# Optimization experiments

Measured on AMD Instinct MI355X. Metric: run time of the kernel, lower is better.

## Reference

```python
import jax, jax.numpy as jnp
import numpy as np

HIDDEN = 1024
HEADS = 16
HEAD_DIM = HIDDEN // HEADS
SCALE = float(np.sqrt(HEAD_DIM))


def setup_inputs() -> dict:
    key = jax.random.key(0)
    ks = jax.random.split(key, 9)
    B, S = 4, 8192
    std = 1.0 / np.sqrt(HIDDEN)
    x = jax.random.normal(ks[0], (B, S, HIDDEN), dtype=jnp.float32)
    Wq = jax.random.normal(ks[1], (HIDDEN, HIDDEN), dtype=jnp.float32) * std
    Wk = jax.random.normal(ks[2], (HIDDEN, HIDDEN), dtype=jnp.float32) * std
    Wv = jax.random.normal(ks[3], (HIDDEN, HIDDEN), dtype=jnp.float32) * std
    Wo = jax.random.normal(ks[4], (HIDDEN, HIDDEN), dtype=jnp.float32) * std
    bq = jax.random.normal(ks[5], (HIDDEN,), dtype=jnp.float32) * std
    bk = jax.random.normal(ks[6], (HIDDEN,), dtype=jnp.float32) * std
    bv = jax.random.normal(ks[7], (HIDDEN,), dtype=jnp.float32) * std
    bo = jax.random.normal(ks[8], (HIDDEN,), dtype=jnp.float32) * std
    return {"x": x, "Wq": Wq, "bq": bq, "Wk": Wk, "bk": bk,
            "Wv": Wv, "bv": bv, "Wo": Wo, "bo": bo}


def reference(x, Wq, bq, Wk, bk, Wv, bv, Wo, bo):
    B, S, E = x.shape
    H, D = HEADS, HEAD_DIM
    # torch nn.Linear: y = x @ W^T + b
    q = (jnp.einsum('bse,fe->bsf', x, Wq) + bq).reshape(B, S, H, D)
    k = (jnp.einsum('bse,fe->bsf', x, Wk) + bk).reshape(B, S, H, D)
    v = (jnp.einsum('bse,fe->bsf', x, Wv) + bv).reshape(B, S, H, D)
    # Faithful to source: NO head transpose, so matmul contracts over head_dim
    # with (B,S) as batch dims -> per-token head-mixing scores [B,S,H,H].
    scores = jnp.einsum('bshd,bsgd->bshg', q, k) / SCALE
    probs = jax.nn.softmax(scores, axis=-1)
    attn = jnp.einsum('bshg,bsgd->bshd', probs, v).reshape(B, S, E)
    return jnp.einsum('bse,fe->bsf', attn, Wo) + bo
```

## Files before the change

kernel.cpp:

```cpp
#include <hip/hip_runtime.h>
#include <hip/hip_bf16.h>
#include <cstdint>
#include <type_traits>

#define GLOBAL_AS __attribute__((address_space(1)))
#define LDS_AS    __attribute__((address_space(3)))

typedef short bf16x8 __attribute__((ext_vector_type(8)));
typedef short short8_t __attribute__((ext_vector_type(8)));
typedef float f32x4  __attribute__((ext_vector_type(4)));

static constexpr int E_DIM = 1024;
static constexpr int HD = 64;
static constexpr int QKV_STRIDE = 3072;
static constexpr int KDIM = 1024;
static constexpr int NTK  = KDIM / 64;
static constexpr int NIT  = NTK / 2;

__device__ __forceinline__ float b2f(short s) {
    union { unsigned u; float f; } x;
    x.u = ((unsigned)(unsigned short)s) << 16;
    return x.f;
}
__device__ __forceinline__ short f2b(float f) {
    union { float f; unsigned u; } x; x.f = f;
    unsigned r = x.u + 0x7FFF + ((x.u >> 16) & 1);
    return (short)(r >> 16);
}

__global__ __launch_bounds__(256) void k_prep(
    const float* __restrict__ x,
    const float* __restrict__ Wq, const float* __restrict__ Wk,
    const float* __restrict__ Wv, const float* __restrict__ Wo,
    const float* __restrict__ bq, const float* __restrict__ bk,
    const float* __restrict__ bv,
    short* __restrict__ xb, short* __restrict__ Wqkvb, short* __restrict__ Wob,
    float* __restrict__ bqkv, int n4x, int n4w)
{
    int i = blockIdx.x * 256 + threadIdx.x;
    const float* src;
    short* dst;
    int j;
    if (i < n4x)                       { src = x;  dst = xb;                  j = i; }
    else if (i < n4x + n4w)            { src = Wq; dst = Wqkvb;               j = i - n4x; }
    else if (i < n4x + 2 * n4w)        { src = Wk; dst = Wqkvb + 4 * n4w;     j = i - n4x - n4w; }
    else if (i < n4x + 3 * n4w)        { src = Wv; dst = Wqkvb + 8 * n4w;     j = i - n4x - 2 * n4w; }
    else if (i < n4x + 4 * n4w)        { src = Wo; dst = Wob;                 j = i - n4x - 3 * n4w; }
    else {
        int b = i - (n4x + 4 * n4w);
        if (b < 768) {
            #pragma unroll
            for (int e = 0; e < 4; ++e) {
                int idx = b * 4 + e;
                float v = (idx < 1024) ? bq[idx] : (idx < 2048 ? bk[idx - 1024] : bv[idx - 2048]);
                bqkv[idx] = v;
            }
        }
        return;
    }
    float4 v = reinterpret_cast<const float4*>(src)[j];
    short4 o;
    o.x = f2b(v.x); o.y = f2b(v.y); o.z = f2b(v.z); o.w = f2b(v.w);
    reinterpret_cast<short4*>(dst)[j] = o;
}

template <typename OutT>
__global__ __launch_bounds__(512, 2) void k_gemm256(
    const short* __restrict__ A,
    const short* __restrict__ Bm,
    const float* __restrict__ bias,
    OutT* __restrict__ C,
    int NT_N, int N)
{
    __shared__ short lds[65536];

    const int tid  = threadIdx.x;
    const int lane = tid & 63;
    const int wv   = tid >> 6;
    const int wr   = wv >> 2;
    const int wc   = wv & 3;
    const int frow = lane & 15;
    const int ks   = lane >> 4;
    const int sw   = frow & 7;
    const int sl0  = ((0 + ks) ^ sw) * 8;
    const int sl1  = ((4 + ks) ^ sw) * 8;

    const int nwg = gridDim.x, nper = nwg >> 3, bid = blockIdx.x;
    const int swz = (bid & 7) * nper + (bid >> 3);
    const int m0  = (swz / NT_N) * 256;
    const int n0  = (swz % NT_N) * 256;

    const int ArdBase = wr * 8192;
    const int BrdBase = 16384 + (wc >> 1) * 8192 + (wc & 1) * 4096;

    const int srow = tid >> 3;
    const int ssl  = ((tid & 7) ^ (srow & 7)) * 8;
    const int sdst = tid * 8;

#define GLD(SRC, DST) __builtin_amdgcn_global_load_lds(                            \
        (const GLOBAL_AS short*)(SRC), (LDS_AS short*)(DST), 16, 0, 0)
#define STAGE_A(BUF, HALF, T) do {                                                 \
    const short* s_ = A + (size_t)(m0 + (HALF) * 128 + srow) * KDIM + (T) * 64 + ssl; \
    short* d_ = &lds[(BUF) * 32768 + (HALF) * 8192 + sdst];                        \
    GLD(s_, d_);  GLD(s_ + (size_t)64 * KDIM, d_ + 4096);                          \
} while (0)
#define STAGE_B(BUF, HALF, T) do {                                                 \
    const short* s_ = Bm + (size_t)(n0 + (HALF) * 128 + srow) * KDIM + (T) * 64 + ssl; \
    short* d_ = &lds[(BUF) * 32768 + 16384 + (HALF) * 8192 + sdst];                \
    GLD(s_, d_);  GLD(s_ + (size_t)64 * KDIM, d_ + 4096);                          \
} while (0)

#define RD_A(BUF, MIB) do {                                                        \
    _Pragma("unroll")                                                              \
    for (int m_ = 0; m_ < 4; ++m_) {                                               \
        const short* p_ = &lds[(BUF) * 32768 + ArdBase + ((MIB) + m_) * 1024 + frow * 64]; \
        af[m_][0] = *(const bf16x8*)(p_ + sl0);                                    \
        af[m_][1] = *(const bf16x8*)(p_ + sl1);                                    \
    }                                                                              \
} while (0)
#define RD_B(BUF, NIB, BF) do {                                                    \
    _Pragma("unroll")                                                              \
    for (int n_ = 0; n_ < 2; ++n_) {                                               \
        const short* p_ = &lds[(BUF) * 32768 + BrdBase + ((NIB) + n_) * 1024 + frow * 64]; \
        BF[n_][0] = *(const bf16x8*)(p_ + sl0);                                    \
        BF[n_][1] = *(const bf16x8*)(p_ + sl1);                                    \
    }                                                                              \
} while (0)

#define MM(MB, NB, BF) do {                                                        \
    _Pragma("unroll")                                                              \
    for (int m_ = 0; m_ < 4; ++m_)                                                 \
        _Pragma("unroll")                                                          \
        for (int n_ = 0; n_ < 2; ++n_) {                                           \
            acc[(MB)+m_][(NB)+n_] = __builtin_amdgcn_mfma_f32_16x16x32_bf16(       \
                af[m_][0], BF[n_][0], acc[(MB)+m_][(NB)+n_], 0, 0, 0);             \
            acc[(MB)+m_][(NB)+n_] = __builtin_amdgcn_mfma_f32_16x16x32_bf16(       \
                af[m_][1], BF[n_][1], acc[(MB)+m_][(NB)+n_], 0, 0, 0);             \
        }                                                                          \
} while (0)

#define BAR   do { __builtin_amdgcn_s_barrier();                                   \
                   __builtin_amdgcn_sched_barrier(0); } while (0)
#define VM8   asm volatile("s_waitcnt vmcnt(8)" ::: "memory")
#define PRIO1 __builtin_amdgcn_s_setprio(1)
#define PRIO0 __builtin_amdgcn_s_setprio(0)

    f32x4 acc[8][4];
    #pragma unroll
    for (int i = 0; i < 8; ++i)
        #pragma unroll
        for (int j = 0; j < 4; ++j)
            acc[i][j] = (f32x4){0.f, 0.f, 0.f, 0.f};

    bf16x8 af[4][2], bfA[2][2], bfB[2][2];

    STAGE_A(0, 0, 0);  STAGE_B(0, 0, 0);  STAGE_B(0, 1, 0);  STAGE_A(0, 1, 0);
    STAGE_B(1, 0, 1);  STAGE_B(1, 1, 1);
    STAGE_A(1, 0, 1);  STAGE_A(1, 1, 1);
    VM8;  BAR;

    #pragma unroll 1
    for (int it = 0; it < NIT; ++it) {
        const int tb = (2 * it + 2 <= 15) ? 2 * it + 2 : 15;
        const int tc = (2 * it + 3 <= 15) ? 2 * it + 3 : 15;
        const int bb = tb & 1, bc = tc & 1;

        RD_A(0, 0);  RD_B(0, 0, bfA);
        BAR;
        PRIO1;  MM(0, 0, bfA);  PRIO0;  BAR;
        RD_B(0, 2, bfB);
        BAR;
        PRIO1;  MM(0, 2, bfB);  PRIO0;  BAR;
        RD_A(0, 4);
        STAGE_B(bb, 0, tb);  STAGE_B(bb, 1, tb);
        BAR;
        PRIO1;  MM(4, 0, bfA);  PRIO0;  BAR;
        STAGE_A(bb, 0, tb);  STAGE_A(bb, 1, tb);
        BAR;
        PRIO1;  MM(4, 2, bfB);  PRIO0;
        VM8;  BAR;

        RD_A(1, 0);  RD_B(1, 0, bfA);
        BAR;
        PRIO1;  MM(0, 0, bfA);  PRIO0;  BAR;
        RD_B(1, 2, bfB);
        BAR;
        PRIO1;  MM(0, 2, bfB);  PRIO0;  BAR;
        RD_A(1, 4);
        STAGE_B(bc, 0, tc);  STAGE_B(bc, 1, tc);
        BAR;
        PRIO1;  MM(4, 0, bfA);  PRIO0;  BAR;
        STAGE_A(bc, 0, tc);  STAGE_A(bc, 1, tc);
        BAR;
        PRIO1;  MM(4, 2, bfB);  PRIO0;
        VM8;  BAR;
    }

    asm volatile("s_waitcnt vmcnt(0)" ::: "memory");

    const int crow = (lane >> 4) * 4;
    const int ccol = lane & 15;
    float bv4[4];
    #pragma unroll
    for (int ni = 0; ni < 4; ++ni)
        bv4[ni] = bias[n0 + wc * 64 + ni * 16 + ccol];
    #pragma unroll
    for (int mi = 0; mi < 8; ++mi) {
        #pragma unroll
        for (int r = 0; r < 4; ++r) {
            const size_t rowg = (size_t)(m0 + wr * 128 + mi * 16 + crow + r) * N;
            #pragma unroll
            for (int ni = 0; ni < 4; ++ni) {
                const int col = n0 + wc * 64 + ni * 16 + ccol;
                float v = acc[mi][ni][r] + bv4[ni];
                if constexpr (std::is_same<OutT, float>::value) {
                    C[rowg + col] = v;
                } else {
                    C[rowg + col] = f2b(v);
                }
            }
        }
    }
#undef GLD
#undef STAGE_A
#undef STAGE_B
#undef RD_A
#undef RD_B
#undef MM
#undef BAR
#undef VM8
#undef PRIO1
#undef PRIO0
}

__global__ __launch_bounds__(256) void k_attn(
    const short* __restrict__ QKV, short* __restrict__ O)
{
    __shared__ short Ks[16][1032];
    __shared__ short Vs[16][1032];

    const int tid = threadIdx.x;
    const int tok0 = blockIdx.x * 16;

    for (int i = tid; i < 2048; i += 256) {
        int t = i >> 7;
        int j = i & 127;
        const size_t base = (size_t)(tok0 + t) * QKV_STRIDE;
        *reinterpret_cast<short8_t*>(&Ks[t][j * 8]) =
            *reinterpret_cast<const short8_t*>(&QKV[base + 1024 + j * 8]);
        *reinterpret_cast<short8_t*>(&Vs[t][j * 8]) =
            *reinterpret_cast<const short8_t*>(&QKV[base + 2048 + j * 8]);
    }
    __syncthreads();

    const int tl = tid >> 4;
    const int h  = tid & 15;

    float qf[64];
    const short* qp = QKV + (size_t)(tok0 + tl) * QKV_STRIDE + h * HD;
    #pragma unroll
    for (int i = 0; i < 8; ++i) {
        short8_t v = *reinterpret_cast<const short8_t*>(&qp[i * 8]);
        #pragma unroll
        for (int j = 0; j < 8; ++j) qf[i * 8 + j] = b2f(v[j]);
    }

    float s[16];
    #pragma unroll
    for (int g = 0; g < 16; ++g) {
        float a = 0.f;
        #pragma unroll
        for (int i = 0; i < 8; ++i) {
            short8_t kv = *reinterpret_cast<const short8_t*>(&Ks[tl][g * HD + i * 8]);
            #pragma unroll
            for (int j = 0; j < 8; ++j) a += qf[i * 8 + j] * b2f(kv[j]);
        }
        s[g] = a * 0.125f;
    }
    float mx = s[0];
    #pragma unroll
    for (int g = 1; g < 16; ++g) mx = fmaxf(mx, s[g]);
    float l = 0.f;
    #pragma unroll
    for (int g = 0; g < 16; ++g) { s[g] = __expf(s[g] - mx); l += s[g]; }
    const float inv = 1.f / l;
    #pragma unroll
    for (int g = 0; g < 16; ++g) s[g] *= inv;

    short* op = O + (size_t)(tok0 + tl) * E_DIM + h * HD;
    #pragma unroll
    for (int c = 0; c < 4; ++c) {
        float a[16];
        #pragma unroll
        for (int j = 0; j < 16; ++j) a[j] = 0.f;
        #pragma unroll
        for (int g = 0; g < 16; ++g) {
            short8_t v0 = *reinterpret_cast<const short8_t*>(&Vs[tl][g * HD + c * 16]);
            short8_t v1 = *reinterpret_cast<const short8_t*>(&Vs[tl][g * HD + c * 16 + 8]);
            #pragma unroll
            for (int j = 0; j < 8; ++j) {
                a[j]     += s[g] * b2f(v0[j]);
                a[8 + j] += s[g] * b2f(v1[j]);
            }
        }
        short8_t o0, o1;
        #pragma unroll
        for (int j = 0; j < 8; ++j) { o0[j] = f2b(a[j]); o1[j] = f2b(a[8 + j]); }
        *reinterpret_cast<short8_t*>(&op[c * 16])     = o0;
        *reinterpret_cast<short8_t*>(&op[c * 16 + 8]) = o1;
    }
}

extern "C" void kernel_launch(void* const* d_in, const int* in_sizes, int n_in,
                              void* d_out, int out_size, void* d_ws, size_t ws_size,
                              hipStream_t stream) {
    const float* x  = (const float*)d_in[0];
    const float* Wq = (const float*)d_in[1];
    const float* bq = (const float*)d_in[2];
    const float* Wk = (const float*)d_in[3];
    const float* bk = (const float*)d_in[4];
    const float* Wv = (const float*)d_in[5];
    const float* bv = (const float*)d_in[6];
    const float* Wo = (const float*)d_in[7];
    const float* bo = (const float*)d_in[8];
    float* out = (float*)d_out;

    const int T = in_sizes[0] / E_DIM;
    char* ws = (char*)d_ws;
    const size_t SZ_X    = (size_t)T * E_DIM * 2;
    const size_t SZ_WQKV = (size_t)3 * E_DIM * E_DIM * 2;
    const size_t SZ_W    = (size_t)E_DIM * E_DIM * 2;
    const size_t SZ_B    = 3072 * sizeof(float) + 4096;

    short* xb    = (short*)(ws);
    short* Wqkvb = (short*)(ws + SZ_X);
    short* Wob   = (short*)(ws + SZ_X + SZ_WQKV);
    float* bqkv  = (float*)(ws + SZ_X + SZ_WQKV + SZ_W);
    short* QKVb  = (short*)(ws + SZ_X + SZ_WQKV + SZ_W + SZ_B);
    short* Ab    = xb;

    const int n4x = T * E_DIM / 4;
    const int n4w = E_DIM * E_DIM / 4;
    const int nprep = n4x + 4 * n4w + 768;
    k_prep<<<dim3((nprep + 255) / 256), dim3(256), 0, stream>>>(
        x, Wq, Wk, Wv, Wo, bq, bk, bv, xb, Wqkvb, Wob, bqkv, n4x, n4w);

    k_gemm256<short><<<dim3((T / 256) * (QKV_STRIDE / 256)), dim3(512), 0, stream>>>(
        xb, Wqkvb, bqkv, QKVb, QKV_STRIDE / 256, QKV_STRIDE);

    k_attn<<<dim3(T / 16), dim3(256), 0, stream>>>(QKVb, Ab);

    k_gemm256<float><<<dim3((T / 256) * (E_DIM / 256)), dim3(512), 0, stream>>>(
        Ab, Wob, bo, out, E_DIM / 256, E_DIM);
}
```

Baseline: 407.6 us.

## Restagger GEMM global-to-LDS prefetch schedule with finer-grained waitcnt control

Reorders the GEMM main loop so A tiles are staged one step later and interleaved with B staging across the four MFMA phases, reducing outstanding loads from 8 to 4 per sync point. Removes sched_barrier from BAR and adds explicit lgkmcnt waits so LDS reads can overlap with barriers. The aim is to spread memory traffic more evenly across compute phases and cut stall time at barriers. In exchange, the compiler gets more scheduling freedom and the hand-tuned buffer-reuse ordering must stay race-free.

```diff
diff --git a/kernel.cpp b/kernel.cpp
--- a/kernel.cpp
+++ b/kernel.cpp
@@ -139,9 +139,10 @@
         }                                                                          \
 } while (0)
 
-#define BAR   do { __builtin_amdgcn_s_barrier();                                   \
-                   __builtin_amdgcn_sched_barrier(0); } while (0)
-#define VM8   asm volatile("s_waitcnt vmcnt(8)" ::: "memory")
+#define BAR   __builtin_amdgcn_s_barrier()
+#define LGKM0 asm volatile("s_waitcnt lgkmcnt(0)")
+#define LGKM8 asm volatile("s_waitcnt lgkmcnt(8)")
+#define VM4   asm volatile("s_waitcnt vmcnt(4)" ::: "memory")
 #define PRIO1 __builtin_amdgcn_s_setprio(1)
 #define PRIO0 __builtin_amdgcn_s_setprio(0)
 
@@ -154,46 +155,50 @@
 
     bf16x8 af[4][2], bfA[2][2], bfB[2][2];
 
-    STAGE_A(0, 0, 0);  STAGE_B(0, 0, 0);  STAGE_B(0, 1, 0);  STAGE_A(0, 1, 0);
+    STAGE_B(0, 0, 0);  STAGE_B(0, 1, 0);
+    STAGE_A(0, 0, 0);  STAGE_A(0, 1, 0);
     STAGE_B(1, 0, 1);  STAGE_B(1, 1, 1);
-    STAGE_A(1, 0, 1);  STAGE_A(1, 1, 1);
-    VM8;  BAR;
+    VM4;  BAR;
 
     #pragma unroll 1
     for (int it = 0; it < NIT; ++it) {
+        const int ta = 2 * it + 1;
         const int tb = (2 * it + 2 <= 15) ? 2 * it + 2 : 15;
         const int tc = (2 * it + 3 <= 15) ? 2 * it + 3 : 15;
-        const int bb = tb & 1, bc = tc & 1;
 
         RD_A(0, 0);  RD_B(0, 0, bfA);
-        BAR;
+        STAGE_A(1, 0, ta);
+        LGKM8;  BAR;  LGKM0;
         PRIO1;  MM(0, 0, bfA);  PRIO0;  BAR;
         RD_B(0, 2, bfB);
-        BAR;
+        STAGE_A(1, 1, ta);
+        BAR;  LGKM0;
         PRIO1;  MM(0, 2, bfB);  PRIO0;  BAR;
         RD_A(0, 4);
-        STAGE_B(bb, 0, tb);  STAGE_B(bb, 1, tb);
-        BAR;
+        STAGE_B(0, 0, tb);
+        BAR;  LGKM0;
         PRIO1;  MM(4, 0, bfA);  PRIO0;  BAR;
-        STAGE_A(bb, 0, tb);  STAGE_A(bb, 1, tb);
+        STAGE_B(0, 1, tb);
         BAR;
         PRIO1;  MM(4, 2, bfB);  PRIO0;
-        VM8;  BAR;
+        VM4;  BAR;
 
         RD_A(1, 0);  RD_B(1, 0, bfA);
-        BAR;
+        STAGE_A(0, 0, tb);
+        LGKM8;  BAR;  LGKM0;
         PRIO1;  MM(0, 0, bfA);  PRIO0;  BAR;
         RD_B(1, 2, bfB);
-        BAR;
+        STAGE_A(0, 1, tb);
+        BAR;  LGKM0;
         PRIO1;  MM(0, 2, bfB);  PRIO0;  BAR;
         RD_A(1, 4);
-        STAGE_B(bc, 0, tc);  STAGE_B(bc, 1, tc);
-        BAR;
+        STAGE_B(1, 0, tc);
+        BAR;  LGKM0;
         PRIO1;  MM(4, 0, bfA);  PRIO0;  BAR;
-        STAGE_A(bc, 0, tc);  STAGE_A(bc, 1, tc);
+        STAGE_B(1, 1, tc);
         BAR;
         PRIO1;  MM(4, 2, bfB);  PRIO0;
-        VM8;  BAR;
+        VM4;  BAR;
     }
 
     asm volatile("s_waitcnt vmcnt(0)" ::: "memory");
@@ -228,7 +233,9 @@
 #undef RD_B
 #undef MM
 #undef BAR
-#undef VM8
+#undef LGKM0
+#undef LGKM8
+#undef VM4
 #undef PRIO1
 #undef PRIO0
 }
```

After: 393.0 us. 1.04x faster.
